# Optimization experiments

Hardware: AMD Instinct MI355X
Metric: run time of the kernel (lower is better)

## Reference

```python
import jax, jax.numpy as jnp
import numpy as np

B, N, DIM = 1, 32768, 512
H, DH = 8, 64            # heads, dim_head
INNER = H * DH           # 512
L = 64                   # n_cluster = clip(N // (16*16) + 1, 16, 64) = 64 landmarks
ITERS = 6                # pinv_iterations
KS = 33                  # residual_conv_kernel


def setup_inputs() -> dict:
    key = jax.random.key(0)
    k1, k2, k3, k4, k5 = jax.random.split(key, 5)
    x = jax.random.normal(k1, (B, N, DIM), jnp.float32)
    labels = jax.random.randint(k2, (N,), 0, L, jnp.int32)  # kmeans cluster ids (no_grad constants)
    Wqkv = jax.random.normal(k3, (DIM, 3 * INNER), jnp.float32) * 0.02
    Wout = jax.random.normal(k4, (INNER, DIM), jnp.float32) * 0.02
    bout = jnp.zeros((DIM,), jnp.float32)
    res_kernel = jax.random.normal(k5, (H, 1, KS, 1), jnp.float32) * 0.05  # depthwise conv, groups=H
    return dict(x=x, Wqkv=Wqkv, Wout=Wout, bout=bout, res_kernel=res_kernel, labels=labels)


def _pinv(a, iters=ITERS):
    # Moore-Penrose via Newton-Schulz, matching moore_penrose_iter_pinv (global max normalization)
    abs_a = jnp.abs(a)
    z = a.swapaxes(-1, -2) / (abs_a.sum(-1).max() * abs_a.sum(-2).max())
    I = jnp.eye(a.shape[-1], dtype=a.dtype)
    for _ in range(iters):
        az = a @ z
        z = 0.25 * z @ (13.0 * I - az @ (15.0 * I - az @ (7.0 * I - az)))
    return z


def _pool_mean(t, seg):
    # ragged per-cluster mean: t [b,h,n,d], seg [n] sorted cluster ids -> [b,h,L,d]
    b, h, n, d = t.shape
    flat = t.transpose(2, 0, 1, 3).reshape(n, b * h * d)
    sums = jax.ops.segment_sum(flat, seg, num_segments=L)
    counts = jax.ops.segment_sum(jnp.ones((n,), t.dtype), seg, num_segments=L)
    means = sums / jnp.maximum(counts, 1.0)[:, None]
    return means.reshape(L, b, h, d).transpose(1, 2, 0, 3)


def reference(x, Wqkv, Wout, bout, res_kernel, labels):
    # cluster sort / unsort (mirrors x[:, index] ... out[:, index_ori])
    index = jnp.argsort(labels)
    index_ori = jnp.argsort(index)
    seg = labels[index]                      # sorted segment ids
    xp = x[:, index]

    qkv = xp @ Wqkv                          # [b,n,3*inner]
    q, k, v = jnp.split(qkv, 3, axis=-1)
    to_bhnd = lambda t: t.reshape(B, N, H, DH).transpose(0, 2, 1, 3)
    q, k, v = to_bhnd(q), to_bhnd(k), to_bhnd(v)

    ql = _pool_mean(q, seg)                  # [b,h,L,d]
    kl = _pool_mean(k, seg)

    # note: original forward never multiplies by self.scale
    attn1 = jax.nn.softmax(jnp.einsum('bhnd,bhld->bhnl', q, kl), axis=-1)   # [b,h,n,L]
    attn2 = jax.nn.softmax(jnp.einsum('bhid,bhjd->bhij', ql, kl), axis=-1)  # [b,h,L,L]
    attn3 = jax.nn.softmax(jnp.einsum('bhld,bhnd->bhln', ql, k), axis=-1)   # [b,h,L,n]

    out = attn1 @ (_pinv(attn2) @ (attn3 @ v))                              # [b,h,n,d]

    # residual depthwise conv over token axis (Conv2d(h,h,(33,1),groups=h))
    res = jax.lax.conv_general_dilated(
        v, res_kernel, window_strides=(1, 1),
        padding=((KS // 2, KS // 2), (0, 0)),
        dimension_numbers=('NCHW', 'OIHW', 'NCHW'),
        feature_group_count=H)
    out = out + res

    out = out.transpose(0, 2, 1, 3).reshape(B, N, INNER)
    out = out @ Wout + bout
    return out[:, index_ori]
```

## Files before the change

### kernel.cpp

```cpp
#include <hip/hip_runtime.h>
#include <hip/hip_bf16.h>

#define N_TOK 32768
#define DIMC  512
#define NH    8
#define DHD   64
#define NL    64
#define KSZ   33
#define QKVC  1536
#define NCHUNK 64

typedef _Float16 f16;
typedef _Float16 f16x8 __attribute__((ext_vector_type(8)));
typedef _Float16 f16x4 __attribute__((ext_vector_type(4)));
typedef _Float16 f16x2 __attribute__((ext_vector_type(2)));
typedef float    f32x4 __attribute__((ext_vector_type(4)));

#define GLOAD_LDS16(gp, lp) \
    __builtin_amdgcn_global_load_lds((const __attribute__((address_space(1))) void*)(gp), \
                                     (__attribute__((address_space(3))) void*)(lp), 16, 0, 0)

__global__ void transpose_k(const float* __restrict__ W, f16* __restrict__ WT, int R, int C) {
    __shared__ float tile[32][33];
    int bx = blockIdx.x * 32, by = blockIdx.y * 32;
    int tx = threadIdx.x, ty = threadIdx.y;
    #pragma unroll
    for (int i = 0; i < 32; i += 8)
        tile[ty + i][tx] = W[(size_t)(by + ty + i) * C + bx + tx];
    __syncthreads();
    #pragma unroll
    for (int i = 0; i < 32; i += 8)
        WT[(size_t)(bx + ty + i) * R + by + tx] = (f16)tile[tx][ty + i];
}

__global__ __launch_bounds__(256) void hist_chunk_k(const int* __restrict__ labels,
                                                    int* __restrict__ counts,
                                                    int* __restrict__ chunkCnt) {
    __shared__ int hloc[NL];
    int t = threadIdx.x, c = blockIdx.x;
    if (t < NL) hloc[t] = 0;
    __syncthreads();
    atomicAdd(&hloc[labels[c * 256 + t]], 1);
    __syncthreads();
    if (t < NL) {
        chunkCnt[c * NL + t] = hloc[t];
        atomicAdd(&counts[t], hloc[t]);
    }
}

__global__ void scan_all_k(const int* __restrict__ chunkCnt, const int* __restrict__ counts,
                           int* __restrict__ baseC, int* __restrict__ baseG) {
    int l = threadIdx.x;
    int gb = 0;
    for (int j = 0; j < l; ++j) gb += counts[j];
    baseG[l] = gb;
    int run = gb;
    for (int c = 0; c < 128; ++c) {
        baseC[c * NL + l] = run;
        run += chunkCnt[c * NL + l];
    }
}

__global__ __launch_bounds__(256) void place_k(const int* __restrict__ labels,
                                               const int* __restrict__ baseC,
                                               int* __restrict__ indexArr) {
    __shared__ int labs[256];
    int t = threadIdx.x, c = blockIdx.x;
    int ii = c * 256 + t;
    int lab = labels[ii];
    labs[t] = lab;
    __syncthreads();
    int rank = 0;
    for (int j = 0; j < 256; ++j)
        rank += (j < t && labs[j] == lab) ? 1 : 0;
    indexArr[baseC[c * NL + lab] + rank] = ii;
}

__global__ __launch_bounds__(256) void gather_cvt_k(const float4* __restrict__ x4,
                                                    const int* __restrict__ indexArr,
                                                    f16x4* __restrict__ xh4) {
    int t = threadIdx.x;
    int row = blockIdx.x * 2 + (t >> 7);
    int c4 = t & 127;
    int j = indexArr[row];
    float4 v = x4[(size_t)j * 128 + c4];
    f16x4 o = { (f16)v.x, (f16)v.y, (f16)v.z, (f16)v.w };
    xh4[(size_t)row * 128 + c4] = o;
}

template<int BNTOT, bool OUT_F32, int NY>
__global__ __launch_bounds__(512, 4) void gemm_k512(const f16* __restrict__ A, const f16* __restrict__ BT,
                                                    void* __restrict__ Cout, const float* __restrict__ bias,
                                                    const int* __restrict__ scatterIdx) {
    constexpr int K = 512;
    constexpr int NKT = K / 32;
    __shared__ f16 As[3][128 * 32];
    __shared__ f16 Bs[3][256 * 32];
    const int t = threadIdx.x;
    const int orig = blockIdx.x + gridDim.x * blockIdx.y;
    constexpr int NWG = 256 * NY;
    constexpr int CPX = NWG / 8;
    const int lin = (orig & 7) * CPX + (orig >> 3);
    const int mBase = (lin / NY) * 128;
    const int nBase = (lin % NY) * 256;
    const int w = t >> 6, lane = t & 63;
    const int wm = w >> 2, wn = w & 3;
    const int lr = lane & 15, lk = lane >> 4;
    const int kc = (lk ^ ((lr >> 1) & 3)) * 8;
    f32x4 acc[4][4];
    #pragma unroll
    for (int m = 0; m < 4; ++m)
        #pragma unroll
        for (int n = 0; n < 4; ++n) acc[m][n] = (f32x4){0.f, 0.f, 0.f, 0.f};

    auto stage = [&](int buf, int kt) {
        {
            int id = t;
            int row = id >> 2, c = id & 3;
            int cg = c ^ ((row >> 1) & 3);
            GLOAD_LDS16(&A[(size_t)(mBase + row) * K + kt * 32 + cg * 8],
                        &As[buf][(size_t)(w * 64) * 8]);
        }
        #pragma unroll
        for (int r = 0; r < 2; ++r) {
            int id = r * 512 + t;
            int row = id >> 2, c = id & 3;
            int cg = c ^ ((row >> 1) & 3);
            GLOAD_LDS16(&BT[(size_t)(nBase + row) * K + kt * 32 + cg * 8],
                        &Bs[buf][(size_t)(r * 512 + w * 64) * 8]);
        }
    };
    auto compute = [&](int buf) {
        f16x8 af[4], bf[4];
        #pragma unroll
        for (int m = 0; m < 4; ++m)
            af[m] = *(const f16x8*)&As[buf][(wm * 64 + m * 16 + lr) * 32 + kc];
        #pragma unroll
        for (int n = 0; n < 4; ++n)
            bf[n] = *(const f16x8*)&Bs[buf][(wn * 64 + n * 16 + lr) * 32 + kc];
        #pragma unroll
        for (int m = 0; m < 4; ++m)
            #pragma unroll
            for (int n = 0; n < 4; ++n)
                acc[m][n] = __builtin_amdgcn_mfma_f32_16x16x32_f16(bf[n], af[m], acc[m][n], 0, 0, 0);
    };

    stage(0, 0);
    asm volatile("" ::: "memory");
    stage(1, 1);
    for (int kt = 0; kt < NKT; ++kt) {
        if (kt < NKT - 1) {
            asm volatile("s_waitcnt vmcnt(3)" ::: "memory");
        } else {
            asm volatile("s_waitcnt vmcnt(0)" ::: "memory");
        }
        __builtin_amdgcn_s_barrier();
        if (kt + 2 < NKT) stage((kt + 2) % 3, kt + 2);
        compute(kt % 3);
    }

    #pragma unroll
    for (int m = 0; m < 4; ++m) {
        int row = mBase + wm * 64 + m * 16 + lr;
        int srow = OUT_F32 ? scatterIdx[row] : row;
        #pragma unroll
        for (int n = 0; n < 4; ++n) {
            int col = nBase + wn * 64 + n * 16 + lk * 4;
            if constexpr (OUT_F32) {
                float4 bv = *(const float4*)&bias[col];
                float4 sv = make_float4(acc[m][n][0] + bv.x, acc[m][n][1] + bv.y,
                                        acc[m][n][2] + bv.z, acc[m][n][3] + bv.w);
                *(float4*)&((float*)Cout)[(size_t)srow * BNTOT + col] = sv;
            } else {
                f16x4 hv = { (f16)acc[m][n][0], (f16)acc[m][n][1],
                             (f16)acc[m][n][2], (f16)acc[m][n][3] };
                *(f16x4*)&((f16*)Cout)[(size_t)srow * BNTOT + col] = hv;
            }
        }
    }
}

__global__ __launch_bounds__(256) void pool_part_k(const f16* __restrict__ qkvh,
                                                   const int* __restrict__ baseG,
                                                   const int* __restrict__ counts,
                                                   float* __restrict__ psum) {
    int l = blockIdx.x, g = blockIdx.y;
    int t = threadIdx.x;
    int c = t & 127, rg = t >> 7;
    int b0 = baseG[l];
    int cnt = counts[l];
    f32x4 a0 = {0.f,0.f,0.f,0.f}, a1 = {0.f,0.f,0.f,0.f};
    for (int p = g * 2 + rg; p < cnt; p += 8) {
        f16x8 v = *(const f16x8*)&qkvh[(size_t)(b0 + p) * QKVC + c * 8];
        a0[0] += (float)v[0]; a0[1] += (float)v[1]; a0[2] += (float)v[2]; a0[3] += (float)v[3];
        a1[0] += (float)v[4]; a1[1] += (float)v[5]; a1[2] += (float)v[6]; a1[3] += (float)v[7];
    }
    __shared__ f32x4 red[2][128][2];
    red[rg][c][0] = a0; red[rg][c][1] = a1;
    __syncthreads();
    if (t < 128) {
        f32x4 s0 = red[0][t][0] + red[1][t][0];
        f32x4 s1 = red[0][t][1] + red[1][t][1];
        size_t o = ((size_t)g * NL + l) * 1024 + t * 8;
        *(f32x4*)&psum[o] = s0;
        *(f32x4*)&psum[o + 4] = s1;
    }
}

__global__ __launch_bounds__(256) void pool_fin_k(const float* __restrict__ psum,
                                                  const int* __restrict__ counts,
                                                  float* __restrict__ ql, float* __restrict__ kl,
                                                  f16* __restrict__ qlh, f16* __restrict__ klh) {
    int l = blockIdx.x;
    int t = threadIdx.x;
    int bse = t * 4;
    float inv = 1.0f / (float)(counts[l] > 0 ? counts[l] : 1);
    f32x4 s = {0.f,0.f,0.f,0.f};
    #pragma unroll
    for (int g = 0; g < 4; ++g)
        s += *(const f32x4*)&psum[((size_t)g * NL + l) * 1024 + bse];
    s *= inv;
    f16x4 hv = { (f16)s[0], (f16)s[1], (f16)s[2], (f16)s[3] };
    if (bse < 512) {
        int h = bse >> 6, d0 = bse & 63;
        size_t o = ((size_t)(h * 64 + l)) * 64 + d0;
        *(f32x4*)&ql[o] = s;
        *(f16x4*)&qlh[o] = hv;
    } else {
        int bb = bse - 512;
        int h = bb >> 6, d0 = bb & 63;
        size_t o = ((size_t)(h * 64 + l)) * 64 + d0;
        *(f32x4*)&kl[o] = s;
        *(f16x4*)&klh[o] = hv;
    }
}

__global__ __launch_bounds__(256) void attn2_k(const float* __restrict__ ql, const float* __restrict__ kl,
                                               float* __restrict__ a_out, float* __restrict__ mrow,
                                               float* __restrict__ mcol) {
    int h = blockIdx.x;
    __shared__ float qs[64][65], ks[64][65], a[64][65];
    __shared__ float red[64][4];
    __shared__ float rowv[64], colv[64];
    int t = threadIdx.x;
    for (int idx = t; idx < 4096; idx += 256) {
        int r = idx >> 6, c = idx & 63;
        qs[r][c] = ql[h * 4096 + idx];
        ks[r][c] = kl[h * 4096 + idx];
    }
    __syncthreads();
    int i = t >> 2, q4 = t & 3, j0 = q4 * 16;
    float o[16];
    #pragma unroll
    for (int jj = 0; jj < 16; ++jj) o[jj] = 0.f;
    for (int d = 0; d < 64; ++d) {
        float qv = qs[i][d];
        #pragma unroll
        for (int jj = 0; jj < 16; ++jj) o[jj] += qv * ks[j0 + jj][d];
    }
    float pmx = o[0];
    #pragma unroll
    for (int jj = 1; jj < 16; ++jj) pmx = fmaxf(pmx, o[jj]);
    red[i][q4] = pmx;
    __syncthreads();
    float rm = fmaxf(fmaxf(red[i][0], red[i][1]), fmaxf(red[i][2], red[i][3]));
    float psum = 0.f;
    #pragma unroll
    for (int jj = 0; jj < 16; ++jj) { o[jj] = expf(o[jj] - rm); psum += o[jj]; }
    __syncthreads();
    red[i][q4] = psum;
    __syncthreads();
    float rs = red[i][0] + red[i][1] + red[i][2] + red[i][3];
    float inv = 1.0f / rs;
    #pragma unroll
    for (int jj = 0; jj < 16; ++jj) { o[jj] *= inv; a[i][j0 + jj] = o[jj]; }
    __syncthreads();
    for (int idx = t; idx < 4096; idx += 256) a_out[h * 4096 + idx] = a[idx >> 6][idx & 63];
    float rsum = 0.f;
    #pragma unroll
    for (int jj = 0; jj < 16; ++jj) rsum += o[jj];
    __syncthreads();
    red[i][q4] = rsum;
    __syncthreads();
    if (q4 == 0) rowv[i] = red[i][0] + red[i][1] + red[i][2] + red[i][3];
    float csum = 0.f;
    #pragma unroll
    for (int jj = 0; jj < 16; ++jj) csum += a[j0 + jj][i];
    __syncthreads();
    red[i][q4] = csum;
    __syncthreads();
    if (q4 == 0) colv[i] = red[i][0] + red[i][1] + red[i][2] + red[i][3];
    __syncthreads();
    if (t == 0) {
        float mr = rowv[0], mc = colv[0];
        for (int j = 1; j < 64; ++j) { mr = fmaxf(mr, rowv[j]); mc = fmaxf(mc, colv[j]); }
        mrow[h] = mr; mcol[h] = mc;
    }
}

__global__ __launch_bounds__(256) void attn3_pinv_k(const f16* __restrict__ qkvh,
                                                    const f16* __restrict__ qlh,
                                                    float* __restrict__ pm, float* __restrict__ ps,
                                                    float* __restrict__ pacc,
                                                    const float* __restrict__ a_g,
                                                    const float* __restrict__ mrow,
                                                    const float* __restrict__ mcol,
                                                    float* __restrict__ zg) {
    union ShU {
        struct { f16 Qls[64 * 64]; f16 Ks[64 * 64]; f16 vT[64 * 72]; f16 Ps[64 * 72]; float fsh[64]; } a3;
        struct { f16 zRh[64][72], zRl[64][72], cRh[64][72], cRl[64][72],
                 Xh[64][72], Xl[64][72], Yh[64][72], Yl[64][72]; } pv;
    };
    __shared__ ShU sh;
    const int t = threadIdx.x;
    const int w = t >> 6, lane = t & 63;
    const int lr = lane & 15;
    const int h = blockIdx.y;

    if (blockIdx.x == 0) {
        const int lk = lane >> 4;
        f16 (&zRh)[64][72] = sh.pv.zRh; f16 (&zRl)[64][72] = sh.pv.zRl;
        f16 (&cRh)[64][72] = sh.pv.cRh; f16 (&cRl)[64][72] = sh.pv.cRl;
        f16 (&Xh)[64][72]  = sh.pv.Xh;  f16 (&Xl)[64][72]  = sh.pv.Xl;
        f16 (&Yh)[64][72]  = sh.pv.Yh;  f16 (&Yl)[64][72]  = sh.pv.Yl;
        float mr = mrow[0], mc = mcol[0];
        #pragma unroll
        for (int k = 1; k < 8; ++k) { mr = fmaxf(mr, mrow[k]); mc = fmaxf(mc, mcol[k]); }
        const float inv0 = 1.0f / (mr * mc);
        for (int idx = t; idx < 4096; idx += 256) {
            int r = idx >> 6, c = idx & 63;
            float zv = a_g[h * 4096 + idx] * inv0;
            f16 hv = (f16)zv;
            zRh[c][r] = hv; zRl[c][r] = (f16)(zv - (float)hv);
        }
        __syncthreads();

        f32x4 po[4];
        auto product = [&](const f16 (*Lh)[72], const f16 (*Ll)[72],
                           const f16 (*Rh)[72], const f16 (*Rl)[72]) {
            #pragma unroll
            for (int n = 0; n < 4; ++n) po[n] = (f32x4){0.f, 0.f, 0.f, 0.f};
            #pragma unroll
            for (int ck = 0; ck < 2; ++ck) {
                f16x8 axh = *(const f16x8*)&Lh[w * 16 + lr][ck * 32 + lk * 8];
                f16x8 axl = *(const f16x8*)&Ll[w * 16 + lr][ck * 32 + lk * 8];
                #pragma unroll
                for (int n = 0; n < 4; ++n) {
                    f16x8 byh = *(const f16x8*)&Rh[n * 16 + lr][ck * 32 + lk * 8];
                    f16x8 byl = *(const f16x8*)&Rl[n * 16 + lr][ck * 32 + lk * 8];
                    po[n] = __builtin_amdgcn_mfma_f32_16x16x32_f16(byh, axh, po[n], 0, 0, 0);
                    po[n] = __builtin_amdgcn_mfma_f32_16x16x32_f16(byl, axh, po[n], 0, 0, 0);
                    po[n] = __builtin_amdgcn_mfma_f32_16x16x32_f16(byh, axl, po[n], 0, 0, 0);
                }
            }
        };

        for (int it = 0; it < 6; ++it) {
            for (int idx = t; idx < 4096; idx += 256) {
                int r = idx >> 6, c = idx & 63;
                float av = a_g[h * 4096 + idx];
                f16 ah = (f16)av;
                Xh[r][c] = ah; Xl[r][c] = (f16)(av - (float)ah);
                float zv = (float)zRh[r][c] + (float)zRl[r][c];
                f16 zh = (f16)zv;
                Yh[c][r] = zh; Yl[c][r] = (f16)(zv - (float)zh);
            }
            __syncthreads();
            product(Xh, Xl, Yh, Yl);
            __syncthreads();
            #pragma unroll
            for (int n = 0; n < 4; ++n)
                #pragma unroll
                for (int j = 0; j < 4; ++j) {
                    int r = w * 16 + lr, c = n * 16 + lk * 4 + j;
                    float v = po[n][j]; f16 hv = (f16)v; f16 lv = (f16)(v - (float)hv);
                    cRh[r][c] = hv; cRl[r][c] = lv;
                    Xh[c][r] = hv;  Xl[c][r] = lv;
                }
            __syncthreads();
            product(cRh, cRl, Xh, Xl);
            #pragma unroll
            for (int n = 0; n < 4; ++n)
                #pragma unroll
                for (int j = 0; j < 4; ++j) {
                    int r = w * 16 + lr, c = n * 16 + lk * 4 + j;
                    float v = 7.f * ((float)cRh[r][c] + (float)cRl[r][c]) - po[n][j];
                    f16 hv = (f16)v;
                    Yh[c][r] = hv; Yl[c][r] = (f16)(v - (float)hv);
                }
            __syncthreads();
            product(cRh, cRl, Yh, Yl);
            #pragma unroll
            for (int n = 0; n < 4; ++n)
                #pragma unroll
                for (int j = 0; j < 4; ++j) {
                    int r = w * 16 + lr, c = n * 16 + lk * 4 + j;
                    float v = 15.f * ((float)cRh[r][c] + (float)cRl[r][c]) - po[n][j];
                    f16 hv = (f16)v;
                    Xh[c][r] = hv; Xl[c][r] = (f16)(v - (float)hv);
                }
            __syncthreads();
            product(zRh, zRl, Xh, Xl);
            #pragma unroll
            for (int n = 0; n < 4; ++n)
                #pragma unroll
                for (int j = 0; j < 4; ++j) {
                    int r = w * 16 + lr, c = n * 16 + lk * 4 + j;
                    float v = 0.25f * (13.f * ((float)zRh[r][c] + (float)zRl[r][c]) - po[n][j]);
                    f16 hv = (f16)v;
                    zRh[r][c] = hv; zRl[r][c] = (f16)(v - (float)hv);
                }
            __syncthreads();
        }
        for (int idx = t; idx < 4096; idx += 256) {
            int r = idx >> 6, c = idx & 63;
            zg[h * 4096 + idx] = (float)zRh[r][c] + (float)zRl[r][c];
        }
        return;
    }

    const int cx = blockIdx.x - 1;
    const int hi = lane >> 4;
    f16* Qls = sh.a3.Qls;
    f16* Ks  = sh.a3.Ks;
    f16* vT  = sh.a3.vT;
    f16* Ps  = sh.a3.Ps;
    float* fsh = sh.a3.fsh;

    #pragma unroll
    for (int pss = 0; pss < 2; ++pss) {
        int q = pss * 256 + t;
        int r = q >> 3, cs = (q & 7) ^ (r & 7);
        GLOAD_LDS16(&qlh[(size_t)h * 4096 + r * 64 + cs * 8], &Qls[(size_t)(pss * 256 + w * 64) * 8]);
    }
    float m_reg = -1e30f, s_reg = 0.f;
    f32x4 accT[4];
    #pragma unroll
    for (int lf = 0; lf < 4; ++lf) accT[lf] = (f32x4){0.f, 0.f, 0.f, 0.f};

    const int vk8 = t & 7, vnn = t >> 3;

    for (int sub = 0; sub < 8; ++sub) {
        const int n0 = cx * 512 + sub * 64;
        __syncthreads();
        #pragma unroll
        for (int pss = 0; pss < 2; ++pss) {
            int q = pss * 256 + t;
            int r = q >> 3, cs = (q & 7) ^ (r & 7);
            GLOAD_LDS16(&qkvh[(size_t)(n0 + r) * QKVC + 512 + h * 64 + cs * 8],
                        &Ks[(size_t)(pss * 256 + w * 64) * 8]);
        }
        #pragma unroll
        for (int p2 = 0; p2 < 2; ++p2) {
            int n = vnn + 32 * p2;
            f16x8 rv = *(const f16x8*)&qkvh[(size_t)(n0 + n) * QKVC + 1024 + h * 64 + vk8 * 8];
            #pragma unroll
            for (int i = 0; i < 8; ++i) {
                int e = i ^ vk8;
                vT[(vk8 * 8 + e) * 72 + n] = rv[e];
            }
        }
        __syncthreads();
        f32x4 c[4];
        #pragma unroll
        for (int kf = 0; kf < 4; ++kf) c[kf] = (f32x4){0.f, 0.f, 0.f, 0.f};
        const int lq = w * 16 + lr;
        #pragma unroll
        for (int ks = 0; ks < 2; ++ks) {
            f16x8 bf = *(const f16x8*)&Qls[lq * 64 + (((ks * 4 + hi) ^ (lq & 7)) * 8)];
            #pragma unroll
            for (int kf = 0; kf < 4; ++kf) {
                int rn = kf * 16 + lr;
                f16x8 af = *(const f16x8*)&Ks[rn * 64 + (((ks * 4 + hi) ^ (rn & 7)) * 8)];
                c[kf] = __builtin_amdgcn_mfma_f32_16x16x32_f16(af, bf, c[kf], 0, 0, 0);
            }
        }
        float tmax = -1e30f;
        #pragma unroll
        for (int kf = 0; kf < 4; ++kf)
            #pragma unroll
            for (int j = 0; j < 4; ++j) tmax = fmaxf(tmax, c[kf][j]);
        tmax = fmaxf(tmax, __shfl_xor(tmax, 16));
        tmax = fmaxf(tmax, __shfl_xor(tmax, 32));
        float newm = fmaxf(m_reg, tmax);
        float fct = __expf(m_reg - newm);
        float psum = 0.f;
        #pragma unroll
        for (int kf = 0; kf < 4; ++kf) {
            f16x4 pk;
            #pragma unroll
            for (int j = 0; j < 4; ++j) {
                float e = __expf(c[kf][j] - newm);
                psum += e;
                pk[j] = (f16)e;
            }
            *(f16x4*)&Ps[lq * 72 + kf * 16 + hi * 4] = pk;
        }
        psum += __shfl_xor(psum, 16);
        psum += __shfl_xor(psum, 32);
        s_reg = s_reg * fct + psum;
        m_reg = newm;
        if (hi == 0) fsh[lq] = fct;
        __syncthreads();
        #pragma unroll
        for (int lf = 0; lf < 4; ++lf) {
            f32x4 fr = *(const f32x4*)&fsh[lf * 16 + hi * 4];
            accT[lf] *= fr;
        }
        #pragma unroll
        for (int ks = 0; ks < 2; ++ks) {
            f16x8 bf = *(const f16x8*)&vT[(w * 16 + lr) * 72 + ks * 32 + hi * 8];
            #pragma unroll
            for (int lf = 0; lf < 4; ++lf) {
                f16x8 af = *(const f16x8*)&Ps[(lf * 16 + lr) * 72 + ks * 32 + hi * 8];
                accT[lf] = __builtin_amdgcn_mfma_f32_16x16x32_f16(af, bf, accT[lf], 0, 0, 0);
            }
        }
    }
    int part = h * NCHUNK + cx;
    if (hi == 0) {
        pm[part * 64 + w * 16 + lr] = m_reg;
        ps[part * 64 + w * 16 + lr] = s_reg;
    }
    #pragma unroll
    for (int lf = 0; lf < 4; ++lf)
        #pragma unroll
        for (int j = 0; j < 4; ++j)
            pacc[((size_t)part * 64 + (lf * 16 + hi * 4 + j)) * 64 + (w * 16 + lr)] = accT[lf][j];
}

__global__ void attn3_merge_k(const float* __restrict__ pm, const float* __restrict__ ps,
                              const float* __restrict__ pacc, float* __restrict__ T) {
    int l = blockIdx.x, h = blockIdx.y, d = threadIdx.x;
    float m = -1e30f;
    for (int c = 0; c < NCHUNK; ++c) m = fmaxf(m, pm[(h * NCHUNK + c) * 64 + l]);
    float s = 0.f, a = 0.f;
    for (int c = 0; c < NCHUNK; ++c) {
        float wgt = __expf(pm[(h * NCHUNK + c) * 64 + l] - m);
        s += ps[(h * NCHUNK + c) * 64 + l] * wgt;
        a += pacc[((size_t)(h * NCHUNK + c) * 64 + l) * 64 + d] * wgt;
    }
    T[(h * 64 + l) * 64 + d] = a / s;
}

__global__ __launch_bounds__(256) void zmatT_fin_k(const float* __restrict__ zg,
                                                   const float* __restrict__ T,
                                                   f16* __restrict__ MthHi, f16* __restrict__ MthLo) {
    const int h = blockIdx.x;
    __shared__ f16 zFh[64][72], zFl[64][72], tCh[64][72], tCl[64][72];
    const int t = threadIdx.x;
    const int w = t >> 6, lane = t & 63;
    const int lr = lane & 15, lk = lane >> 4;
    for (int idx = t; idx < 4096; idx += 256) {
        int r = idx >> 6, c = idx & 63;
        float zv = zg[h * 4096 + idx]; f16 zh = (f16)zv;
        zFh[r][c] = zh; zFl[r][c] = (f16)(zv - (float)zh);
        float tv = T[h * 4096 + idx]; f16 th = (f16)tv;
        tCh[c][r] = th; tCl[c][r] = (f16)(tv - (float)th);
    }
    __syncthreads();
    f32x4 po[4];
    #pragma unroll
    for (int n = 0; n < 4; ++n) po[n] = (f32x4){0.f, 0.f, 0.f, 0.f};
    #pragma unroll
    for (int ck = 0; ck < 2; ++ck) {
        f16x8 axh = *(const f16x8*)&zFh[w * 16 + lr][ck * 32 + lk * 8];
        f16x8 axl = *(const f16x8*)&zFl[w * 16 + lr][ck * 32 + lk * 8];
        #pragma unroll
        for (int n = 0; n < 4; ++n) {
            f16x8 byh = *(const f16x8*)&tCh[n * 16 + lr][ck * 32 + lk * 8];
            f16x8 byl = *(const f16x8*)&tCl[n * 16 + lr][ck * 32 + lk * 8];
            po[n] = __builtin_amdgcn_mfma_f32_16x16x32_f16(byh, axh, po[n], 0, 0, 0);
            po[n] = __builtin_amdgcn_mfma_f32_16x16x32_f16(byl, axh, po[n], 0, 0, 0);
            po[n] = __builtin_amdgcn_mfma_f32_16x16x32_f16(byh, axl, po[n], 0, 0, 0);
        }
    }
    #pragma unroll
    for (int n = 0; n < 4; ++n)
        #pragma unroll
        for (int j = 0; j < 4; ++j) {
            int r = w * 16 + lr, c = n * 16 + lk * 4 + j;
            float v = po[n][j]; f16 hv = (f16)v;
            MthHi[h * 4096 + c * 64 + r] = hv;
            MthLo[h * 4096 + c * 64 + r] = (f16)(v - (float)hv);
        }
}

__global__ __launch_bounds__(256) void attn1_k(const f16* __restrict__ qkvh, const f16* __restrict__ klh,
                                               const f16* __restrict__ MthHi, const f16* __restrict__ MthLo,
                                               const float* __restrict__ resk, f16* __restrict__ Yh) {
    const int h = blockIdx.y;
    const int p0 = blockIdx.x * 128;
    const int t = threadIdx.x;
    const int w = t >> 6, lane = t & 63;
    const int lr = lane & 15, hi = lane >> 4;
    __shared__ f16 QPs[128][72];
    __shared__ f16 Ks[64][72];
    __shared__ f16 Mhi[64][72];
    __shared__ f16 Mlo[64][72];
    __shared__ f16 vt[160][72];

    #pragma unroll
    for (int i = 0; i < 4; ++i) {
        int id = i * 256 + t, row = id >> 3, c8 = id & 7;
        *(f16x8*)&QPs[row][c8 * 8] = *(const f16x8*)&qkvh[(size_t)(p0 + row) * QKVC + h * 64 + c8 * 8];
    }
    #pragma unroll
    for (int i = 0; i < 2; ++i) {
        int id = i * 256 + t, row = id >> 3, c8 = id & 7;
        *(f16x8*)&Ks[row][c8 * 8]  = *(const f16x8*)&klh[h * 4096 + id * 8];
        *(f16x8*)&Mhi[row][c8 * 8] = *(const f16x8*)&MthHi[h * 4096 + id * 8];
        *(f16x8*)&Mlo[row][c8 * 8] = *(const f16x8*)&MthLo[h * 4096 + id * 8];
    }
    for (int id = t; id < 160 * 8; id += 256) {
        int rr = id >> 3, c8 = id & 7;
        int pg = p0 - 16 + rr;
        int4 v = {0, 0, 0, 0};
        if (pg >= 0 && pg < N_TOK)
            v = *(const int4*)&qkvh[(size_t)pg * QKVC + 1024 + h * 64 + c8 * 8];
        *(int4*)&vt[rr][c8 * 8] = v;
    }
    float wk[KSZ];
    #pragma unroll
    for (int k = 0; k < KSZ; ++k) wk[k] = resk[h * KSZ + k];
    __syncthreads();

    f32x4 c[4][2];
    #pragma unroll
    for (int lf = 0; lf < 4; ++lf)
        #pragma unroll
        for (int nf = 0; nf < 2; ++nf) c[lf][nf] = (f32x4){0.f, 0.f, 0.f, 0.f};
    #pragma unroll
    for (int ks = 0; ks < 2; ++ks) {
        f16x8 af[4], bf[2];
        #pragma unroll
        for (int lf = 0; lf < 4; ++lf) af[lf] = *(const f16x8*)&Ks[lf * 16 + lr][ks * 32 + hi * 8];
        #pragma unroll
        for (int nf = 0; nf < 2; ++nf) bf[nf] = *(const f16x8*)&QPs[w * 32 + nf * 16 + lr][ks * 32 + hi * 8];
        #pragma unroll
        for (int lf = 0; lf < 4; ++lf)
            #pragma unroll
            for (int nf = 0; nf < 2; ++nf)
                c[lf][nf] = __builtin_amdgcn_mfma_f32_16x16x32_f16(af[lf], bf[nf], c[lf][nf], 0, 0, 0);
    }

    #pragma unroll
    for (int nf = 0; nf < 2; ++nf) {
        float m = -1e30f;
        #pragma unroll
        for (int lf = 0; lf < 4; ++lf)
            #pragma unroll
            for (int j = 0; j < 4; ++j) m = fmaxf(m, c[lf][nf][j]);
        m = fmaxf(m, __shfl_xor(m, 16));
        m = fmaxf(m, __shfl_xor(m, 32));
        float s = 0.f;
        #pragma unroll
        for (int lf = 0; lf < 4; ++lf)
            #pragma unroll
            for (int j = 0; j < 4; ++j) { float e = __expf(c[lf][nf][j] - m); c[lf][nf][j] = e; s += e; }
        s += __shfl_xor(s, 16);
        s += __shfl_xor(s, 32);
        float inv = 1.0f / s;
        #pragma unroll
        for (int lf = 0; lf < 4; ++lf) {
            f16x4 pk;
            #pragma unroll
            for (int j = 0; j < 4; ++j) pk[j] = (f16)(c[lf][nf][j] * inv);
            *(f16x4*)&QPs[w * 32 + nf * 16 + lr][lf * 16 + hi * 4] = pk;
        }
    }

    f32x4 o[2][4];
    #pragma unroll
    for (int nf = 0; nf < 2; ++nf)
        #pragma unroll
        for (int df = 0; df < 4; ++df) o[nf][df] = (f32x4){0.f, 0.f, 0.f, 0.f};
    #pragma unroll
    for (int ks = 0; ks < 2; ++ks) {
        f16x8 pa[2], bh[4], bl[4];
        #pragma unroll
        for (int nf = 0; nf < 2; ++nf) pa[nf] = *(const f16x8*)&QPs[w * 32 + nf * 16 + lr][ks * 32 + hi * 8];
        #pragma unroll
        for (int df = 0; df < 4; ++df) {
            bh[df] = *(const f16x8*)&Mhi[df * 16 + lr][ks * 32 + hi * 8];
            bl[df] = *(const f16x8*)&Mlo[df * 16 + lr][ks * 32 + hi * 8];
        }
        #pragma unroll
        for (int nf = 0; nf < 2; ++nf)
            #pragma unroll
            for (int df = 0; df < 4; ++df) {
                o[nf][df] = __builtin_amdgcn_mfma_f32_16x16x32_f16(pa[nf], bh[df], o[nf][df], 0, 0, 0);
                o[nf][df] = __builtin_amdgcn_mfma_f32_16x16x32_f16(pa[nf], bl[df], o[nf][df], 0, 0, 0);
            }
    }

    #pragma unroll
    for (int nf = 0; nf < 2; ++nf)
        #pragma unroll
        for (int df = 0; df < 4; ++df)
            #pragma unroll
            for (int j = 0; j < 4; ++j)
                QPs[w * 32 + nf * 16 + hi * 4 + j][df * 16 + lr] = (f16)(o[nf][df][j]);
    __syncthreads();

    const int d2 = t & 31, rg8 = t >> 5;
    const int r0 = rg8 * 16;
    float c0[48], c1[48];
    #pragma unroll
    for (int j = 0; j < 48; ++j) {
        f16x2 v = *(const f16x2*)&vt[r0 + j][d2 * 2];
        c0[j] = (float)v[0]; c1[j] = (float)v[1];
    }
    #pragma unroll
    for (int pp = 0; pp < 16; ++pp) {
        float a0 = 0.f, a1 = 0.f;
        #pragma unroll
        for (int k = 0; k < KSZ; ++k) { a0 += wk[k] * c0[pp + k]; a1 += wk[k] * c1[pp + k]; }
        int row = r0 + pp;
        f16x2 qv = *(const f16x2*)&QPs[row][d2 * 2];
        f16x2 ov;
        ov[0] = (f16)(a0 + (float)qv[0]);
        ov[1] = (f16)(a1 + (float)qv[1]);
        *(f16x2*)&Yh[(size_t)(p0 + row) * 512 + h * 64 + d2 * 2] = ov;
    }
}

extern "C" void kernel_launch(void* const* d_in, const int* in_sizes, int n_in,
                              void* d_out, int out_size, void* d_ws, size_t ws_size,
                              hipStream_t stream) {
    const float* x    = (const float*)d_in[0];
    const float* Wqkv = (const float*)d_in[1];
    const float* Wout = (const float*)d_in[2];
    const float* bout = (const float*)d_in[3];
    const float* resk = (const float*)d_in[4];
    const int*   labels = (const int*)d_in[5];
    float* out = (float*)d_out;

    char* w = (char*)d_ws;
    size_t off = 0;
    auto alloc = [&](size_t bytes) {
        void* p = w + off;
        off += (bytes + 255) & ~(size_t)255;
        return p;
    };
    f16* xh     = (f16*)alloc((size_t)N_TOK * DIMC * 2);
    f16* qkvh   = (f16*)alloc((size_t)N_TOK * QKVC * 2);
    f16* WqkvT  = (f16*)alloc((size_t)QKVC * DIMC * 2);
    f16* WoutT  = (f16*)alloc((size_t)DIMC * DIMC * 2);
    f16* Yh     = (f16*)alloc((size_t)N_TOK * DIMC * 2);
    int* counts = (int*)alloc(NL * 4);
    int* chunkCnt = (int*)alloc((size_t)128 * NL * 4);
    int* baseC  = (int*)alloc((size_t)128 * NL * 4);
    int* baseG  = (int*)alloc(NL * 4);
    int* indexA = (int*)alloc((size_t)N_TOK * 4);
    float* ql   = (float*)alloc((size_t)NH * 64 * 64 * 4);
    float* kl   = (float*)alloc((size_t)NH * 64 * 64 * 4);
    f16* qlh    = (f16*)alloc((size_t)NH * 64 * 64 * 2);
    f16* klh    = (f16*)alloc((size_t)NH * 64 * 64 * 2);
    float* a2   = (float*)alloc((size_t)NH * 64 * 64 * 4);
    float* mrow = (float*)alloc(NH * 4);
    float* mcol = (float*)alloc(NH * 4);
    float* Tb   = (float*)alloc((size_t)NH * 64 * 64 * 4);
    float* zg   = (float*)alloc((size_t)NH * 64 * 64 * 4);
    f16* MthHi  = (f16*)alloc((size_t)NH * 64 * 64 * 2);
    f16* MthLo  = (f16*)alloc((size_t)NH * 64 * 64 * 2);
    float* pm   = (float*)alloc((size_t)NH * NCHUNK * 64 * 4);
    float* ps   = (float*)alloc((size_t)NH * NCHUNK * 64 * 4);
    float* pacc = (float*)alloc((size_t)NH * NCHUNK * 64 * 64 * 4);
    float* psum = (float*)alloc((size_t)4 * NL * 1024 * 4);

    hipMemsetAsync(counts, 0, NL * 4, stream);

    hist_chunk_k<<<128, 256, 0, stream>>>(labels, counts, chunkCnt);
    scan_all_k<<<1, 64, 0, stream>>>(chunkCnt, counts, baseC, baseG);
    place_k<<<128, 256, 0, stream>>>(labels, baseC, indexA);
    gather_cvt_k<<<N_TOK / 2, 256, 0, stream>>>((const float4*)x, indexA, (f16x4*)xh);
    transpose_k<<<dim3(QKVC / 32, DIMC / 32), dim3(32, 8), 0, stream>>>(Wqkv, WqkvT, DIMC, QKVC);
    transpose_k<<<dim3(DIMC / 32, DIMC / 32), dim3(32, 8), 0, stream>>>(Wout, WoutT, DIMC, DIMC);
    gemm_k512<QKVC, false, 6><<<dim3(N_TOK / 128, QKVC / 256), 512, 0, stream>>>(xh, WqkvT, qkvh, nullptr, nullptr);
    pool_part_k<<<dim3(NL, 4), 256, 0, stream>>>(qkvh, baseG, counts, psum);
    pool_fin_k<<<NL, 256, 0, stream>>>(psum, counts, ql, kl, qlh, klh);
    attn2_k<<<NH, 256, 0, stream>>>(ql, kl, a2, mrow, mcol);
    attn3_pinv_k<<<dim3(NCHUNK + 1, NH), 256, 0, stream>>>(qkvh, qlh, pm, ps, pacc, a2, mrow, mcol, zg);
    attn3_merge_k<<<dim3(NL, NH), 64, 0, stream>>>(pm, ps, pacc, Tb);
    zmatT_fin_k<<<NH, 256, 0, stream>>>(zg, Tb, MthHi, MthLo);
    attn1_k<<<dim3(N_TOK / 128, NH), 256, 0, stream>>>(qkvh, klh, MthHi, MthLo, resk, Yh);
    gemm_k512<DIMC, true, 2><<<dim3(N_TOK / 128, DIMC / 256), 512, 0, stream>>>(Yh, WoutT, out, bout, indexA);
}
```

Before: 297.4 us.

## Fold scan kernel into place and pool kernels; split conv register window

Removes the single-block scan kernel. Each place_k block now computes its per-label base offsets directly from the counts and chunk histograms, and pool_part_k recomputes its segment start from the counts. This saves one serial launch at the cost of redundant prefix sums in every block. Separately, the residual-conv epilogue of attn1_k now processes 16 rows as two halves of 8 with a 40-element window instead of 48, lowering register pressure at the cost of reloading overlapping LDS rows.

```diff
diff --git a/kernel.cpp b/kernel.cpp
--- a/kernel.cpp
+++ b/kernel.cpp
@@ -48,32 +48,27 @@
     }
 }
 
-__global__ void scan_all_k(const int* __restrict__ chunkCnt, const int* __restrict__ counts,
-                           int* __restrict__ baseC, int* __restrict__ baseG) {
-    int l = threadIdx.x;
-    int gb = 0;
-    for (int j = 0; j < l; ++j) gb += counts[j];
-    baseG[l] = gb;
-    int run = gb;
-    for (int c = 0; c < 128; ++c) {
-        baseC[c * NL + l] = run;
-        run += chunkCnt[c * NL + l];
-    }
-}
-
 __global__ __launch_bounds__(256) void place_k(const int* __restrict__ labels,
-                                               const int* __restrict__ baseC,
+                                               const int* __restrict__ counts,
+                                               const int* __restrict__ chunkCnt,
                                                int* __restrict__ indexArr) {
     __shared__ int labs[256];
+    __shared__ int baseL[NL];
     int t = threadIdx.x, c = blockIdx.x;
     int ii = c * 256 + t;
     int lab = labels[ii];
     labs[t] = lab;
+    if (t < NL) {
+        int b = 0;
+        for (int j = 0; j < t; ++j) b += counts[j];
+        for (int cc = 0; cc < c; ++cc) b += chunkCnt[cc * NL + t];
+        baseL[t] = b;
+    }
     __syncthreads();
     int rank = 0;
     for (int j = 0; j < 256; ++j)
         rank += (j < t && labs[j] == lab) ? 1 : 0;
-    indexArr[baseC[c * NL + lab] + rank] = ii;
+    indexArr[baseL[lab] + rank] = ii;
 }
 
 __global__ __launch_bounds__(256) void gather_cvt_k(const float4* __restrict__ x4,
@@ -181,13 +176,13 @@
 }
 
 __global__ __launch_bounds__(256) void pool_part_k(const f16* __restrict__ qkvh,
-                                                   const int* __restrict__ baseG,
                                                    const int* __restrict__ counts,
                                                    float* __restrict__ psum) {
     int l = blockIdx.x, g = blockIdx.y;
     int t = threadIdx.x;
     int c = t & 127, rg = t >> 7;
-    int b0 = baseG[l];
+    int b0 = 0;
+    for (int j = 0; j < l; ++j) b0 += counts[j];
     int cnt = counts[l];
     f32x4 a0 = {0.f,0.f,0.f,0.f}, a1 = {0.f,0.f,0.f,0.f};
     for (int p = g * 2 + rg; p < cnt; p += 8) {
@@ -704,24 +699,27 @@
     __syncthreads();
 
     const int d2 = t & 31, rg8 = t >> 5;
-    const int r0 = rg8 * 16;
-    float c0[48], c1[48];
-    #pragma unroll
-    for (int j = 0; j < 48; ++j) {
-        f16x2 v = *(const f16x2*)&vt[r0 + j][d2 * 2];
-        c0[j] = (float)v[0]; c1[j] = (float)v[1];
-    }
-    #pragma unroll
-    for (int pp = 0; pp < 16; ++pp) {
-        float a0 = 0.f, a1 = 0.f;
-        #pragma unroll
-        for (int k = 0; k < KSZ; ++k) { a0 += wk[k] * c0[pp + k]; a1 += wk[k] * c1[pp + k]; }
-        int row = r0 + pp;
-        f16x2 qv = *(const f16x2*)&QPs[row][d2 * 2];
-        f16x2 ov;
-        ov[0] = (f16)(a0 + (float)qv[0]);
-        ov[1] = (f16)(a1 + (float)qv[1]);
-        *(f16x2*)&Yh[(size_t)(p0 + row) * 512 + h * 64 + d2 * 2] = ov;
+    #pragma unroll
+    for (int half = 0; half < 2; ++half) {
+        const int r0 = rg8 * 16 + half * 8;
+        float c0[40], c1[40];
+        #pragma unroll
+        for (int j = 0; j < 40; ++j) {
+            f16x2 v = *(const f16x2*)&vt[r0 + j][d2 * 2];
+            c0[j] = (float)v[0]; c1[j] = (float)v[1];
+        }
+        #pragma unroll
+        for (int pp = 0; pp < 8; ++pp) {
+            float a0 = 0.f, a1 = 0.f;
+            #pragma unroll
+            for (int k = 0; k < KSZ; ++k) { a0 += wk[k] * c0[pp + k]; a1 += wk[k] * c1[pp + k]; }
+            int row = r0 + pp;
+            f16x2 qv = *(const f16x2*)&QPs[row][d2 * 2];
+            f16x2 ov;
+            ov[0] = (f16)(a0 + (float)qv[0]);
+            ov[1] = (f16)(a1 + (float)qv[1]);
+            *(f16x2*)&Yh[(size_t)(p0 + row) * 512 + h * 64 + d2 * 2] = ov;
+        }
     }
 }
 
@@ -750,8 +748,6 @@
     f16* Yh     = (f16*)alloc((size_t)N_TOK * DIMC * 2);
     int* counts = (int*)alloc(NL * 4);
     int* chunkCnt = (int*)alloc((size_t)128 * NL * 4);
-    int* baseC  = (int*)alloc((size_t)128 * NL * 4);
-    int* baseG  = (int*)alloc(NL * 4);
     int* indexA = (int*)alloc((size_t)N_TOK * 4);
     float* ql   = (float*)alloc((size_t)NH * 64 * 64 * 4);
     float* kl   = (float*)alloc((size_t)NH * 64 * 64 * 4);
@@ -772,13 +768,12 @@
     hipMemsetAsync(counts, 0, NL * 4, stream);
 
     hist_chunk_k<<<128, 256, 0, stream>>>(labels, counts, chunkCnt);
-    scan_all_k<<<1, 64, 0, stream>>>(chunkCnt, counts, baseC, baseG);
-    place_k<<<128, 256, 0, stream>>>(labels, baseC, indexA);
+    place_k<<<128, 256, 0, stream>>>(labels, counts, chunkCnt, indexA);
     gather_cvt_k<<<N_TOK / 2, 256, 0, stream>>>((const float4*)x, indexA, (f16x4*)xh);
     transpose_k<<<dim3(QKVC / 32, DIMC / 32), dim3(32, 8), 0, stream>>>(Wqkv, WqkvT, DIMC, QKVC);
     transpose_k<<<dim3(DIMC / 32, DIMC / 32), dim3(32, 8), 0, stream>>>(Wout, WoutT, DIMC, DIMC);
     gemm_k512<QKVC, false, 6><<<dim3(N_TOK / 128, QKVC / 256), 512, 0, stream>>>(xh, WqkvT, qkvh, nullptr, nullptr);
-    pool_part_k<<<dim3(NL, 4), 256, 0, stream>>>(qkvh, baseG, counts, psum);
+    pool_part_k<<<dim3(NL, 4), 256, 0, stream>>>(qkvh, counts, psum);
     pool_fin_k<<<NL, 256, 0, stream>>>(psum, counts, ql, kl, qlh, klh);
     attn2_k<<<NH, 256, 0, stream>>>(ql, kl, a2, mrow, mcol);
     attn3_pinv_k<<<dim3(NCHUNK + 1, NH), 256, 0, stream>>>(qkvh, qlh, pm, ps, pacc, a2, mrow, mcol, zg);
```

Result: slower. 309.8 us (+4.2%).
